# Kernel tuning notes

Hardware: AMD Instinct MI355X
Metric: run time of the kernel (lower is better)

Reference implementation:

```python
import jax, jax.numpy as jnp
import numpy as np

B, L, D, HD, DC = 2, 2048, 2048, 64, 2048
NH = D // HD  # 32 heads


def _rms_norm(x, eps):
    return x * jax.lax.rsqrt(jnp.mean(jnp.square(x), axis=-1, keepdims=True) + eps)


def _apply_rope(x, rope):
    # x: [b,h,l,d]; rope: [2,l,d]. x_hat = interleave(-x_odd, x_even)
    x2 = x.reshape(*x.shape[:-1], HD // 2, 2)
    x_hat = jnp.stack([-x2[..., 1], x2[..., 0]], axis=-1).reshape(x.shape)
    return x * rope[0] + x_hat * rope[1]


def setup_inputs() -> dict:
    key = jax.random.key(0)
    ks = jax.random.split(key, 6)
    return {
        "x": jax.random.normal(ks[0], (B, L, D), jnp.float32),
        "condition": jax.random.normal(ks[1], (B, DC), jnp.float32),
        "rope": jax.random.normal(ks[2], (2, L, HD), jnp.float32),
        "w_ada": jax.random.normal(ks[3], (2 * D, DC), jnp.float32) * 0.02,
        "w_qkv": jax.random.normal(ks[4], (3 * D, D), jnp.float32) * 0.02,
        "w_out": jax.random.normal(ks[5], (D, D), jnp.float32) * 0.02,
        "qk_w": jnp.ones((HD,), jnp.float32),
    }


def reference(x, condition, rope, w_ada, w_qkv, w_out, qk_w):
    eps = jnp.finfo(x.dtype).eps
    # AdaRMSNorm
    ss = (condition @ w_ada.T)[:, None, :]          # [b,1,2D]
    shift, scale = jnp.split(ss, 2, axis=-1)
    h = _rms_norm(x, eps) * (1.0 + scale) + shift   # [b,l,D]
    # fused QKV projection: 'b l (n h d)'
    qkv = (h @ w_qkv.T).reshape(B, L, 3, NH, HD)
    qkv = jnp.transpose(qkv, (2, 0, 3, 1, 4))       # [3,b,h,l,d]
    q, k, v = qkv[0], qkv[1], qkv[2]
    # per-head RMSNorm (with affine weight) + RoPE
    q = _apply_rope(_rms_norm(q, eps) * qk_w, rope)
    k = _apply_rope(_rms_norm(k, eps) * qk_w, rope)
    # SDPA
    scores = jnp.einsum('bhqd,bhkd->bhqk', q, k) / jnp.sqrt(jnp.asarray(HD, x.dtype))
    attn = jax.nn.softmax(scores, axis=-1)
    o = jnp.einsum('bhqk,bhkd->bhqd', attn, v)      # [b,h,l,d]
    o = jnp.transpose(o, (0, 2, 1, 3)).reshape(B, L, D)
    return o @ w_out.T
```

## Files before the change

### kernel.cpp

```cpp
#include <hip/hip_runtime.h>


typedef __bf16 bf16x8 __attribute__((ext_vector_type(8)));
typedef float  f32x4  __attribute__((ext_vector_type(4)));
typedef float  f32x16 __attribute__((ext_vector_type(16)));

#define EPS_F32 1.1920929e-07f
#define QSCALE 0.18033688011112042f

#if defined(__has_builtin)
#  if __has_builtin(__builtin_amdgcn_exp2f)
#    define EXP2F(x) __builtin_amdgcn_exp2f(x)
#  else
#    define EXP2F(x) __expf((x) * 0.6931471805599453f)
#  endif
#  if __has_builtin(__builtin_amdgcn_rcpf)
#    define RCPF(x) __builtin_amdgcn_rcpf(x)
#  else
#    define RCPF(x) (1.0f / (x))
#  endif
#else
#  define EXP2F(x) __expf((x) * 0.6931471805599453f)
#  define RCPF(x) (1.0f / (x))
#endif

__device__ __forceinline__ float bf2f(unsigned int u16) {
  union { unsigned int i; float f; } v; v.i = (u16 & 0xffffu) << 16; return v.f;
}
__device__ __forceinline__ unsigned short f2bf(float f) {
  union { float f; unsigned int i; } v; v.f = f;
  unsigned int r = v.i + 0x7fffu + ((v.i >> 16) & 1u);
  return (unsigned short)(r >> 16);
}
__device__ __forceinline__ unsigned int f2bf_rn_u(float f) {
  union { float f; unsigned int i; } v; v.f = f;
  return v.i + 0x8000u;
}

__device__ __forceinline__ void gload16(const void* g, void* l) {
  __builtin_amdgcn_global_load_lds(
      (const __attribute__((address_space(1))) unsigned int*)(unsigned long long)g,
      (__attribute__((address_space(3))) unsigned int*)(unsigned int)(unsigned long long)l,
      16, 0, 0);
}

__global__ __launch_bounds__(256) void ada_gemm_kernel(
    const float* __restrict__ cond, const float* __restrict__ w_ada,
    float* __restrict__ ss)
{
  const int lane = threadIdx.x & 63;
  const int gw = blockIdx.x * 4 + (threadIdx.x >> 6);
  const int b = gw >> 12;
  const int j = gw & 4095;
  const float4* wr = (const float4*)(w_ada + j * 2048);
  const float4* cr = (const float4*)(cond + b * 2048);
  float acc = 0.f;
  #pragma unroll
  for (int k4 = 0; k4 < 8; ++k4) {
    float4 w = wr[lane + k4 * 64];
    float4 c = cr[lane + k4 * 64];
    acc += w.x * c.x + w.y * c.y + w.z * c.z + w.w * c.w;
  }
  #pragma unroll
  for (int off = 1; off < 64; off <<= 1) acc += __shfl_xor(acc, off);
  if (lane == 0) ss[b * 4096 + j] = acc;
}

__global__ __launch_bounds__(256) void ada_rms_kernel(
    const float* __restrict__ x, const float* __restrict__ ss,
    unsigned short* __restrict__ H)
{
  const int row = blockIdx.x;
  const int b = row >> 11;
  const int tid = threadIdx.x;
  const int lane = tid & 63, wave = tid >> 6;
  const float* xr = x + (size_t)row * 2048;
  float4 v0 = ((const float4*)xr)[tid * 2];
  float4 v1 = ((const float4*)xr)[tid * 2 + 1];
  float ssq = v0.x*v0.x + v0.y*v0.y + v0.z*v0.z + v0.w*v0.w
            + v1.x*v1.x + v1.y*v1.y + v1.z*v1.z + v1.w*v1.w;
  #pragma unroll
  for (int off = 1; off < 64; off <<= 1) ssq += __shfl_xor(ssq, off);
  __shared__ float red[4];
  if (lane == 0) red[wave] = ssq;
  __syncthreads();
  const float tot = red[0] + red[1] + red[2] + red[3];
  const float r = rsqrtf(tot * (1.f / 2048.f) + EPS_F32);
  const int c0 = tid * 8;
  const float* sh = ss + b * 4096;
  float xv[8] = {v0.x, v0.y, v0.z, v0.w, v1.x, v1.y, v1.z, v1.w};
  unsigned int pk[4];
  #pragma unroll
  for (int p = 0; p < 4; ++p) {
    const int c = c0 + p * 2;
    float h0 = xv[p*2+0] * r * (1.f + sh[2048 + c])     + sh[c];
    float h1 = xv[p*2+1] * r * (1.f + sh[2048 + c + 1]) + sh[c + 1];
    pk[p] = (unsigned int)f2bf(h0) | ((unsigned int)f2bf(h1) << 16);
  }
  *(uint4*)&H[(size_t)row * 2048 + c0] = make_uint4(pk[0], pk[1], pk[2], pk[3]);
}

__global__ __launch_bounds__(256) void cast2_kernel(
    const float* __restrict__ a,
    const float* __restrict__ b,
    unsigned short* __restrict__ dst)
{
  const int i = blockIdx.x * 256 + threadIdx.x;
  float4 v = (i < 3145728) ? ((const float4*)a)[i]
                           : ((const float4*)b)[i - 3145728];
  unsigned int p0 = (unsigned int)f2bf(v.x) | ((unsigned int)f2bf(v.y) << 16);
  unsigned int p1 = (unsigned int)f2bf(v.z) | ((unsigned int)f2bf(v.w) << 16);
  *(uint2*)&dst[(size_t)i * 4] = make_uint2(p0, p1);
}

__global__ __launch_bounds__(512, 2) void gemm_qkv_8p(
    const unsigned short* __restrict__ A,
    const unsigned short* __restrict__ Bw,
    unsigned short* __restrict__ C,
    unsigned short* __restrict__ vt,
    const float* __restrict__ rope,
    const float* __restrict__ qk_w)
{
  __shared__ unsigned short As[2][2][8192];
  __shared__ unsigned short Bs[2][2][8192];

  const int tid  = threadIdx.x;
  const int lane = tid & 63;
  const int wave = tid >> 6;
  const int wrow = (wave >> 2) * 128;
  const int wcol = (wave & 3) * 64;

  const int swz = (blockIdx.x & 7) * 48 + (blockIdx.x >> 3);
  const int bx = swz >> 4;
  const int by = swz & 15;
  const int bm = by * 256;
  const int bn = bx * 256;

  const int fr = lane & 15;
  const int q_ = lane >> 4;
  const int laneoff = fr * 32 + ((q_ ^ ((fr >> 1) & 3)) << 3);

  const int rA  = wave * 32 + (lane >> 2);
  const int kk  = (lane & 3) ^ ((lane >> 3) & 3);
  const unsigned short* Ag0 = A  + (size_t)(bm + rA) * 2048 + kk * 8;
  const unsigned short* Ag1 = Ag0 + (size_t)16 * 2048;
  const unsigned short* Bg0 = Bw + (size_t)(bn + rA) * 2048 + kk * 8;
  const unsigned short* Bg1 = Bg0 + (size_t)16 * 2048;
  const int ldso = rA * 32 + (lane & 3) * 8;

  f32x4 acc[8][4] = {};
  bf16x8 fA[4], fB[4];

#define STAGE_A(SB, SKH, KT) do { \
    gload16(Ag0 + (KT) * 64 + (SKH) * 32, &As[SB][SKH][ldso]); \
    gload16(Ag1 + (KT) * 64 + (SKH) * 32, &As[SB][SKH][ldso + 512]); } while (0)
#define STAGE_B(SB, SKH, KT) do { \
    gload16(Bg0 + (KT) * 64 + (SKH) * 32, &Bs[SB][SKH][ldso]); \
    gload16(Bg1 + (KT) * 64 + (SKH) * 32, &Bs[SB][SKH][ldso + 512]); } while (0)
#define VMW(N) asm volatile("s_waitcnt vmcnt(" #N ")" ::: "memory")
#define LDB(BUF, KH) do { const unsigned short* p_ = &Bs[BUF][KH][wcol * 32 + laneoff]; \
    fB[0] = *(const bf16x8*)&p_[0];    fB[1] = *(const bf16x8*)&p_[512]; \
    fB[2] = *(const bf16x8*)&p_[1024]; fB[3] = *(const bf16x8*)&p_[1536]; } while (0)
#define LDA(BUF, KH, MH) do { const unsigned short* p_ = &As[BUF][KH][(wrow + (MH) * 64) * 32 + laneoff]; \
    fA[0] = *(const bf16x8*)&p_[0];    fA[1] = *(const bf16x8*)&p_[512]; \
    fA[2] = *(const bf16x8*)&p_[1024]; fA[3] = *(const bf16x8*)&p_[1536]; } while (0)
#define MFMA16(MH) do { \
    _Pragma("unroll") \
    for (int f_ = 0; f_ < 4; ++f_) { \
      _Pragma("unroll") \
      for (int n_ = 0; n_ < 4; ++n_) \
        acc[(MH) * 4 + f_][n_] = __builtin_amdgcn_mfma_f32_16x16x32_bf16( \
            fA[f_], fB[n_], acc[(MH) * 4 + f_][n_], 0, 0, 0); \
    } } while (0)
#define PH_MID() do { __builtin_amdgcn_s_barrier(); \
    asm volatile("s_waitcnt lgkmcnt(0)"); \
    __builtin_amdgcn_s_setprio(1); } while (0)
#define PH_END() do { __builtin_amdgcn_s_setprio(0); \
    __builtin_amdgcn_s_barrier(); } while (0)

  STAGE_A(0, 0, 0); STAGE_B(0, 0, 0); STAGE_A(0, 1, 0); STAGE_B(0, 1, 0);
  VMW(4);
  __builtin_amdgcn_s_barrier();

  for (int it = 0; it < 16; ++it) {
    const int t1 = 2 * it + 1;
    const int t2 = 2 * it + 2;
    const bool pf = (it < 15);

    LDB(0, 0); LDA(0, 0, 0);
    STAGE_A(1, 0, t1);
    PH_MID(); MFMA16(0); PH_END();
    LDA(0, 0, 1);
    STAGE_B(1, 0, t1);
    VMW(4);
    PH_MID(); MFMA16(1); PH_END();
    LDB(0, 1); LDA(0, 1, 0);
    STAGE_A(1, 1, t1);
    PH_MID(); MFMA16(0); PH_END();
    LDA(0, 1, 1);
    STAGE_B(1, 1, t1);
    VMW(4);
    PH_MID(); MFMA16(1); PH_END();

    LDB(1, 0); LDA(1, 0, 0);
    if (pf) STAGE_A(0, 0, t2);
    PH_MID(); MFMA16(0); PH_END();
    LDA(1, 0, 1);
    if (pf) { STAGE_B(0, 0, t2); VMW(4); }
    else    { VMW(0); }
    PH_MID(); MFMA16(1); PH_END();
    LDB(1, 1); LDA(1, 1, 0);
    if (pf) STAGE_A(0, 1, t2);
    PH_MID(); MFMA16(0); PH_END();
    LDA(1, 1, 1);
    if (pf) STAGE_B(0, 1, t2);
    VMW(4);
    PH_MID(); MFMA16(1); PH_END();
  }

#undef STAGE_A
#undef STAGE_B
#undef VMW
#undef LDB
#undef LDA
#undef MFMA16
#undef PH_MID
#undef PH_END

  const int cr = (lane >> 4) * 4;
  const int cc = lane & 15;
  if (bn >= 4096) {
    #pragma unroll
    for (int mf = 0; mf < 8; ++mf)
      #pragma unroll
      for (int nf = 0; nf < 4; ++nf)
        #pragma unroll
        for (int r = 0; r < 4; ++r) {
          const int m  = bm + wrow + mf * 16 + cr + r;
          const int dg = bn + wcol + nf * 16 + cc - 4096;
          const int l  = m & 2047;
          const size_t dst = ((size_t)((m >> 11) * 32 + (dg >> 6)) * 64 + (dg & 63)) * 2048
                           + (l >> 6) * 64 + (l & 15) * 4 + ((l >> 4) & 3);
          vt[dst] = f2bf(acc[mf][nf][r]);
        }
  } else {
    const bool is_q = (bn + wcol) < 2048;
    const float qs = is_q ? QSCALE : 1.0f;
    float w4[4];
    #pragma unroll
    for (int nf = 0; nf < 4; ++nf) w4[nf] = qk_w[nf * 16 + cc];
    #pragma unroll
    for (int mf = 0; mf < 8; ++mf)
      #pragma unroll
      for (int r = 0; r < 4; ++r) {
        const int row = bm + wrow + mf * 16 + cr + r;
        const int l = row & 2047;
        float ssq = 0.f;
        #pragma unroll
        for (int nf = 0; nf < 4; ++nf) { const float v = acc[mf][nf][r]; ssq += v * v; }
        ssq += __shfl_xor(ssq, 1);
        ssq += __shfl_xor(ssq, 2);
        ssq += __shfl_xor(ssq, 4);
        ssq += __shfl_xor(ssq, 8);
        const float rn = rsqrtf(ssq * (1.f / 64.f) + EPS_F32) * qs;
        const float* rp0 = rope + l * 64 + cc;
        const float* rp1 = rp0 + 131072;
        #pragma unroll
        for (int nf = 0; nf < 4; ++nf) {
          const float vn = acc[mf][nf][r] * rn * w4[nf];
          const float vp = __shfl_xor(vn, 1);
          const float vh = (cc & 1) ? vp : -vp;
          const float o = vn * rp0[nf * 16] + vh * rp1[nf * 16];
          C[(size_t)row * 6144 + bn + wcol + nf * 16 + cc] = f2bf(o);
        }
      }
  }
}

__global__ __launch_bounds__(512, 1) void gemm_out_4p(
    const unsigned short* __restrict__ A,
    const unsigned short* __restrict__ Bw,
    float* __restrict__ C)
{
  __shared__ unsigned short As[2][2][8192];
  __shared__ unsigned short Bs[2][2][4096];

  const int tid  = threadIdx.x;
  const int lane = tid & 63;
  const int wave = tid >> 6;
  const int wrow = (wave >> 1) * 64;
  const int wcol = (wave & 1) * 64;

  const int swz = (blockIdx.x & 7) * 32 + (blockIdx.x >> 3);
  const int bx = swz >> 4;
  const int by = swz & 15;
  const int bm = by * 256;
  const int bn = bx * 128;

  const int fr = lane & 15;
  const int q_ = lane >> 4;
  const int laneoff = fr * 32 + ((q_ ^ ((fr >> 1) & 3)) << 3);

  const int rA = wave * 32 + (lane >> 2);
  const int rB = wave * 16 + (lane >> 2);
  const int kk = (lane & 3) ^ ((lane >> 3) & 3);
  const unsigned short* Ag0 = A  + (size_t)(bm + rA) * 2048 + kk * 8;
  const unsigned short* Ag1 = Ag0 + (size_t)16 * 2048;
  const unsigned short* Bg0 = Bw + (size_t)(bn + rB) * 2048 + kk * 8;
  const int ldsoA = rA * 32 + (lane & 3) * 8;
  const int ldsoB = rB * 32 + (lane & 3) * 8;

  f32x4 acc[4][4] = {};
  bf16x8 fA[4], fB[4];

#define STAGE_A4(SB, SKH, KT) do { \
    gload16(Ag0 + (KT) * 64 + (SKH) * 32, &As[SB][SKH][ldsoA]); \
    gload16(Ag1 + (KT) * 64 + (SKH) * 32, &As[SB][SKH][ldsoA + 512]); } while (0)
#define STAGE_B4(SB, SKH, KT) \
    gload16(Bg0 + (KT) * 64 + (SKH) * 32, &Bs[SB][SKH][ldsoB])
#define VMW(N) asm volatile("s_waitcnt vmcnt(" #N ")" ::: "memory")
#define LDB4(BUF, KH) do { const unsigned short* p_ = &Bs[BUF][KH][wcol * 32 + laneoff]; \
    fB[0] = *(const bf16x8*)&p_[0];    fB[1] = *(const bf16x8*)&p_[512]; \
    fB[2] = *(const bf16x8*)&p_[1024]; fB[3] = *(const bf16x8*)&p_[1536]; } while (0)
#define LDA4(BUF, KH) do { const unsigned short* p_ = &As[BUF][KH][wrow * 32 + laneoff]; \
    fA[0] = *(const bf16x8*)&p_[0];    fA[1] = *(const bf16x8*)&p_[512]; \
    fA[2] = *(const bf16x8*)&p_[1024]; fA[3] = *(const bf16x8*)&p_[1536]; } while (0)
#define MFMA16_4() do { \
    _Pragma("unroll") \
    for (int f_ = 0; f_ < 4; ++f_) { \
      _Pragma("unroll") \
      for (int n_ = 0; n_ < 4; ++n_) \
        acc[f_][n_] = __builtin_amdgcn_mfma_f32_16x16x32_bf16( \
            fA[f_], fB[n_], acc[f_][n_], 0, 0, 0); \
    } } while (0)
#define PH_MID() do { __builtin_amdgcn_s_barrier(); \
    asm volatile("s_waitcnt lgkmcnt(0)"); \
    __builtin_amdgcn_s_setprio(1); } while (0)
#define PH_END() do { __builtin_amdgcn_s_setprio(0); \
    __builtin_amdgcn_s_barrier(); } while (0)

  STAGE_A4(0, 0, 0); STAGE_B4(0, 0, 0);
  STAGE_A4(0, 1, 0); STAGE_B4(0, 1, 0);
  VMW(3);
  __builtin_amdgcn_s_barrier();

  for (int it = 0; it < 16; ++it) {
    const int t1 = 2 * it + 1;
    const int t2 = 2 * it + 2;
    const bool pf = (it < 15);

    LDB4(0, 0); LDA4(0, 0);
    STAGE_A4(1, 0, t1); STAGE_B4(1, 0, t1);
    VMW(3);
    PH_MID(); MFMA16_4(); PH_END();
    LDB4(0, 1); LDA4(0, 1);
    STAGE_A4(1, 1, t1); STAGE_B4(1, 1, t1);
    VMW(3);
    PH_MID(); MFMA16_4(); PH_END();

    LDB4(1, 0); LDA4(1, 0);
    if (pf) { STAGE_A4(0, 0, t2); STAGE_B4(0, 0, t2); VMW(3); }
    else    { VMW(0); }
    PH_MID(); MFMA16_4(); PH_END();
    LDB4(1, 1); LDA4(1, 1);
    if (pf) { STAGE_A4(0, 1, t2); STAGE_B4(0, 1, t2); VMW(3); }
    else    { VMW(0); }
    PH_MID(); MFMA16_4(); PH_END();
  }

#undef STAGE_A4
#undef STAGE_B4
#undef VMW
#undef LDB4
#undef LDA4
#undef MFMA16_4
#undef PH_MID
#undef PH_END

  const int cr = (lane >> 4) * 4;
  const int cc = lane & 15;
  #pragma unroll
  for (int f = 0; f < 4; ++f)
    #pragma unroll
    for (int n = 0; n < 4; ++n)
      #pragma unroll
      for (int r = 0; r < 4; ++r) {
        const int row = bm + wrow + f * 16 + cr + r;
        const int col = bn + wcol + n * 16 + cc;
        C[(size_t)row * 2048 + col] = acc[f][n][r];
      }
}

__global__ __launch_bounds__(256, 2) void attn_mfma_kernel(
    const unsigned short* __restrict__ QKV,
    const unsigned short* __restrict__ Vt,
    unsigned short* __restrict__ O)
{
  __shared__ unsigned short Ks[64 * 72];
  __shared__ unsigned short Vs[64 * 72];
  __shared__ unsigned short Ps[4 * 64 * 68];
  const int tid  = threadIdx.x;
  const int lane = tid & 63;
  const int wave = tid >> 6;
  const int blk = blockIdx.x;
  const int bh = blk & 63;
  const int qt = blk >> 6;
  const int b = bh >> 5, h = bh & 31;
  const int rowbase = b << 11;
  const int qbase = qt * 256 + wave * 64;

  const int m16  = lane & 15;
  const int quad = lane >> 4;
  const int m32  = lane & 31;
  const int hl   = lane >> 5;

  bf16x8 qf[4][2];
  #pragma unroll
  for (int qi = 0; qi < 4; ++qi)
    #pragma unroll
    for (int ch = 0; ch < 2; ++ch)
      qf[qi][ch] = *(const bf16x8*)&QKV[(size_t)(rowbase + qbase + qi * 16 + m16) * 6144
                                        + h * 64 + ch * 32 + quad * 8];

  const int sr = tid >> 2;
  const int sc = (tid & 3) * 16;
  const unsigned short* Kg = QKV + (size_t)(rowbase + sr) * 6144 + 2048 + h * 64 + sc;
  const unsigned short* Vg = Vt + (size_t)(bh * 64 + sr) * 2048 + sc;

  f32x16 accO[2][2] = {};
  float part[4][4] = {};
  unsigned short* Pw = &Ps[(wave * 64) * 68];

  for (int kt = 0; kt < 32; ++kt) {
    __syncthreads();
    {
      const uint4* kp = (const uint4*)(Kg + (size_t)kt * 64 * 6144);
      const uint4* vp = (const uint4*)(Vg + kt * 64);
      uint4 k0 = kp[0], k1 = kp[1];
      uint4 v0 = vp[0], v1 = vp[1];
      *(uint4*)&Ks[sr * 72 + sc]     = k0;
      *(uint4*)&Ks[sr * 72 + sc + 8] = k1;
      *(uint4*)&Vs[sr * 72 + sc]     = v0;
      *(uint4*)&Vs[sr * 72 + sc + 8] = v1;
    }
    __syncthreads();

    unsigned int pk[4][4][2];
    #pragma unroll
    for (int kj = 0; kj < 4; ++kj) {
      bf16x8 kf0 = *(const bf16x8*)&Ks[(kj * 16 + m16) * 72 + quad * 8];
      bf16x8 kf1 = *(const bf16x8*)&Ks[(kj * 16 + m16) * 72 + 32 + quad * 8];
      #pragma unroll
      for (int qi = 0; qi < 4; ++qi) {
        f32x4 acc = {};
        acc = __builtin_amdgcn_mfma_f32_16x16x32_bf16(qf[qi][0], kf0, acc, 0, 0, 0);
        acc = __builtin_amdgcn_mfma_f32_16x16x32_bf16(qf[qi][1], kf1, acc, 0, 0, 0);
        #pragma unroll
        for (int r = 0; r < 4; ++r) {
          float p = EXP2F(acc[r]);
          part[qi][r] += p;
          unsigned int pb = f2bf_rn_u(p);
          if (kj == 0)      pk[qi][r][0]  = pb >> 16;
          else if (kj == 1) pk[qi][r][0] |= pb & 0xffff0000u;
          else if (kj == 2) pk[qi][r][1]  = pb >> 16;
          else              pk[qi][r][1] |= pb & 0xffff0000u;
        }
      }
    }
    #pragma unroll
    for (int qi = 0; qi < 4; ++qi)
      #pragma unroll
      for (int r = 0; r < 4; ++r)
        *(uint2*)&Pw[(qi * 16 + quad * 4 + r) * 68 + m16 * 4] =
            make_uint2(pk[qi][r][0], pk[qi][r][1]);

    #pragma unroll
    for (int ch = 0; ch < 4; ++ch) {
      bf16x8 pa0 = *(const bf16x8*)&Pw[m32 * 68 + ch * 16 + hl * 8];
      bf16x8 pa1 = *(const bf16x8*)&Pw[(32 + m32) * 68 + ch * 16 + hl * 8];
      bf16x8 vb0 = *(const bf16x8*)&Vs[m32 * 72 + ch * 16 + hl * 8];
      bf16x8 vb1 = *(const bf16x8*)&Vs[(32 + m32) * 72 + ch * 16 + hl * 8];
      accO[0][0] = __builtin_amdgcn_mfma_f32_32x32x16_bf16(pa0, vb0, accO[0][0], 0, 0, 0);
      accO[0][1] = __builtin_amdgcn_mfma_f32_32x32x16_bf16(pa0, vb1, accO[0][1], 0, 0, 0);
      accO[1][0] = __builtin_amdgcn_mfma_f32_32x32x16_bf16(pa1, vb0, accO[1][0], 0, 0, 0);
      accO[1][1] = __builtin_amdgcn_mfma_f32_32x32x16_bf16(pa1, vb1, accO[1][1], 0, 0, 0);
    }
  }

  #pragma unroll
  for (int qi = 0; qi < 4; ++qi)
    #pragma unroll
    for (int r = 0; r < 4; ++r)
      #pragma unroll
      for (int off = 1; off < 16; off <<= 1)
        part[qi][r] += __shfl_xor(part[qi][r], off);

  #pragma unroll
  for (int qs = 0; qs < 2; ++qs) {
    #pragma unroll
    for (int reg = 0; reg < 16; ++reg) {
      const int r = reg & 3;
      const int s = reg >> 2;
      const int qsrc = ((2 * s + hl) & 3) * 16 + m16;
      const float rs = __shfl(part[qs * 2 + (reg >> 3)][r], qsrc);
      const float inv = RCPF(rs);
      const int rho = r + 8 * s + 4 * hl;
      const size_t base = (size_t)(rowbase + qbase + qs * 32 + rho) * 2048 + h * 64;
      O[base + m32]      = f2bf(accO[qs][0][reg] * inv);
      O[base + 32 + m32] = f2bf(accO[qs][1][reg] * inv);
    }
  }
}

extern "C" void kernel_launch(void* const* d_in, const int* in_sizes, int n_in,
                              void* d_out, int out_size, void* d_ws, size_t ws_size,
                              hipStream_t stream) {
  (void)in_sizes; (void)n_in; (void)out_size; (void)ws_size;
  const float* x     = (const float*)d_in[0];
  const float* cond  = (const float*)d_in[1];
  const float* rope  = (const float*)d_in[2];
  const float* w_ada = (const float*)d_in[3];
  const float* w_qkv = (const float*)d_in[4];
  const float* w_out = (const float*)d_in[5];
  const float* qk_w  = (const float*)d_in[6];
  float* out = (float*)d_out;

  char* ws = (char*)d_ws;
  float*          ss   = (float*)ws;
  unsigned short* H    = (unsigned short*)(ws + 32768);
  unsigned short* Wq   = H + 8388608;
  unsigned short* Wo   = Wq + 12582912;
  unsigned short* QKV  = Wo + 4194304;
  unsigned short* Vt_g = QKV + 25165824;

  ada_gemm_kernel<<<2048, 256, 0, stream>>>(cond, w_ada, ss);
  ada_rms_kernel<<<4096, 256, 0, stream>>>(x, ss, H);
  cast2_kernel<<<16384, 256, 0, stream>>>(w_qkv, w_out, Wq);
  gemm_qkv_8p<<<384, 512, 0, stream>>>(H, Wq, QKV, Vt_g, rope, qk_w);
  attn_mfma_kernel<<<512, 256, 0, stream>>>(QKV, Vt_g, H);
  gemm_out_4p<<<256, 512, 0, stream>>>(H, Wo, out);
}
```

Measured before the change: 447.6 us.

## Split QKV GEMM into 256x128 tiles and move QK norm+RoPE to separate kernel

Replaces the 256x256-tile QKV GEMM (two blocks per CU) with a 256x128-tile variant modeled on the out-projection kernel, launched with 768 blocks and a rescaled swizzle. The per-head RMSNorm, qk weight, scale and RoPE epilogue is moved out of the GEMM into a new elementwise kernel that rewrites Q and K in place. The goal is more blocks and a lighter GEMM epilogue, at the cost of an extra launch and an extra read and write of Q and K. Q/K are normalized from bf16-rounded values rather than fp32 accumulators, which slightly changes numerics.

Result: no change. 443.7 us (-0.9%).

```diff
diff --git a/kernel.cpp b/kernel.cpp
--- a/kernel.cpp
+++ b/kernel.cpp
@@ -27,6 +27,9 @@
 __device__ __forceinline__ float bf2f(unsigned int u16) {
   union { unsigned int i; float f; } v; v.i = (u16 & 0xffffu) << 16; return v.f;
 }
+__device__ __forceinline__ float bf2f_hi(unsigned int u32) {
+  union { unsigned int i; float f; } v; v.i = u32 & 0xffff0000u; return v.f;
+}
 __device__ __forceinline__ unsigned short f2bf(float f) {
   union { float f; unsigned int i; } v; v.f = f;
   unsigned int r = v.i + 0x7fffu + ((v.i >> 16) & 1u);
@@ -113,174 +116,11 @@
   *(uint2*)&dst[(size_t)i * 4] = make_uint2(p0, p1);
 }
 
-__global__ __launch_bounds__(512, 2) void gemm_qkv_8p(
+__global__ __launch_bounds__(512, 1) void gemm_qkv_4p(
     const unsigned short* __restrict__ A,
     const unsigned short* __restrict__ Bw,
     unsigned short* __restrict__ C,
-    unsigned short* __restrict__ vt,
-    const float* __restrict__ rope,
-    const float* __restrict__ qk_w)
-{
-  __shared__ unsigned short As[2][2][8192];
-  __shared__ unsigned short Bs[2][2][8192];
-
-  const int tid  = threadIdx.x;
-  const int lane = tid & 63;
-  const int wave = tid >> 6;
-  const int wrow = (wave >> 2) * 128;
-  const int wcol = (wave & 3) * 64;
-
-  const int swz = (blockIdx.x & 7) * 48 + (blockIdx.x >> 3);
-  const int bx = swz >> 4;
-  const int by = swz & 15;
-  const int bm = by * 256;
-  const int bn = bx * 256;
-
-  const int fr = lane & 15;
-  const int q_ = lane >> 4;
-  const int laneoff = fr * 32 + ((q_ ^ ((fr >> 1) & 3)) << 3);
-
-  const int rA  = wave * 32 + (lane >> 2);
-  const int kk  = (lane & 3) ^ ((lane >> 3) & 3);
-  const unsigned short* Ag0 = A  + (size_t)(bm + rA) * 2048 + kk * 8;
-  const unsigned short* Ag1 = Ag0 + (size_t)16 * 2048;
-  const unsigned short* Bg0 = Bw + (size_t)(bn + rA) * 2048 + kk * 8;
-  const unsigned short* Bg1 = Bg0 + (size_t)16 * 2048;
-  const int ldso = rA * 32 + (lane & 3) * 8;
-
-  f32x4 acc[8][4] = {};
-  bf16x8 fA[4], fB[4];
-
-#define STAGE_A(SB, SKH, KT) do { \
-    gload16(Ag0 + (KT) * 64 + (SKH) * 32, &As[SB][SKH][ldso]); \
-    gload16(Ag1 + (KT) * 64 + (SKH) * 32, &As[SB][SKH][ldso + 512]); } while (0)
-#define STAGE_B(SB, SKH, KT) do { \
-    gload16(Bg0 + (KT) * 64 + (SKH) * 32, &Bs[SB][SKH][ldso]); \
-    gload16(Bg1 + (KT) * 64 + (SKH) * 32, &Bs[SB][SKH][ldso + 512]); } while (0)
-#define VMW(N) asm volatile("s_waitcnt vmcnt(" #N ")" ::: "memory")
-#define LDB(BUF, KH) do { const unsigned short* p_ = &Bs[BUF][KH][wcol * 32 + laneoff]; \
-    fB[0] = *(const bf16x8*)&p_[0];    fB[1] = *(const bf16x8*)&p_[512]; \
-    fB[2] = *(const bf16x8*)&p_[1024]; fB[3] = *(const bf16x8*)&p_[1536]; } while (0)
-#define LDA(BUF, KH, MH) do { const unsigned short* p_ = &As[BUF][KH][(wrow + (MH) * 64) * 32 + laneoff]; \
-    fA[0] = *(const bf16x8*)&p_[0];    fA[1] = *(const bf16x8*)&p_[512]; \
-    fA[2] = *(const bf16x8*)&p_[1024]; fA[3] = *(const bf16x8*)&p_[1536]; } while (0)
-#define MFMA16(MH) do { \
-    _Pragma("unroll") \
-    for (int f_ = 0; f_ < 4; ++f_) { \
-      _Pragma("unroll") \
-      for (int n_ = 0; n_ < 4; ++n_) \
-        acc[(MH) * 4 + f_][n_] = __builtin_amdgcn_mfma_f32_16x16x32_bf16( \
-            fA[f_], fB[n_], acc[(MH) * 4 + f_][n_], 0, 0, 0); \
-    } } while (0)
-#define PH_MID() do { __builtin_amdgcn_s_barrier(); \
-    asm volatile("s_waitcnt lgkmcnt(0)"); \
-    __builtin_amdgcn_s_setprio(1); } while (0)
-#define PH_END() do { __builtin_amdgcn_s_setprio(0); \
-    __builtin_amdgcn_s_barrier(); } while (0)
-
-  STAGE_A(0, 0, 0); STAGE_B(0, 0, 0); STAGE_A(0, 1, 0); STAGE_B(0, 1, 0);
-  VMW(4);
-  __builtin_amdgcn_s_barrier();
-
-  for (int it = 0; it < 16; ++it) {
-    const int t1 = 2 * it + 1;
-    const int t2 = 2 * it + 2;
-    const bool pf = (it < 15);
-
-    LDB(0, 0); LDA(0, 0, 0);
-    STAGE_A(1, 0, t1);
-    PH_MID(); MFMA16(0); PH_END();
-    LDA(0, 0, 1);
-    STAGE_B(1, 0, t1);
-    VMW(4);
-    PH_MID(); MFMA16(1); PH_END();
-    LDB(0, 1); LDA(0, 1, 0);
-    STAGE_A(1, 1, t1);
-    PH_MID(); MFMA16(0); PH_END();
-    LDA(0, 1, 1);
-    STAGE_B(1, 1, t1);
-    VMW(4);
-    PH_MID(); MFMA16(1); PH_END();
-
-    LDB(1, 0); LDA(1, 0, 0);
-    if (pf) STAGE_A(0, 0, t2);
-    PH_MID(); MFMA16(0); PH_END();
-    LDA(1, 0, 1);
-    if (pf) { STAGE_B(0, 0, t2); VMW(4); }
-    else    { VMW(0); }
-    PH_MID(); MFMA16(1); PH_END();
-    LDB(1, 1); LDA(1, 1, 0);
-    if (pf) STAGE_A(0, 1, t2);
-    PH_MID(); MFMA16(0); PH_END();
-    LDA(1, 1, 1);
-    if (pf) STAGE_B(0, 1, t2);
-    VMW(4);
-    PH_MID(); MFMA16(1); PH_END();
-  }
-
-#undef STAGE_A
-#undef STAGE_B
-#undef VMW
-#undef LDB
-#undef LDA
-#undef MFMA16
-#undef PH_MID
-#undef PH_END
-
-  const int cr = (lane >> 4) * 4;
-  const int cc = lane & 15;
-  if (bn >= 4096) {
-    #pragma unroll
-    for (int mf = 0; mf < 8; ++mf)
-      #pragma unroll
-      for (int nf = 0; nf < 4; ++nf)
-        #pragma unroll
-        for (int r = 0; r < 4; ++r) {
-          const int m  = bm + wrow + mf * 16 + cr + r;
-          const int dg = bn + wcol + nf * 16 + cc - 4096;
-          const int l  = m & 2047;
-          const size_t dst = ((size_t)((m >> 11) * 32 + (dg >> 6)) * 64 + (dg & 63)) * 2048
-                           + (l >> 6) * 64 + (l & 15) * 4 + ((l >> 4) & 3);
-          vt[dst] = f2bf(acc[mf][nf][r]);
-        }
-  } else {
-    const bool is_q = (bn + wcol) < 2048;
-    const float qs = is_q ? QSCALE : 1.0f;
-    float w4[4];
-    #pragma unroll
-    for (int nf = 0; nf < 4; ++nf) w4[nf] = qk_w[nf * 16 + cc];
-    #pragma unroll
-    for (int mf = 0; mf < 8; ++mf)
-      #pragma unroll
-      for (int r = 0; r < 4; ++r) {
-        const int row = bm + wrow + mf * 16 + cr + r;
-        const int l = row & 2047;
-        float ssq = 0.f;
-        #pragma unroll
-        for (int nf = 0; nf < 4; ++nf) { const float v = acc[mf][nf][r]; ssq += v * v; }
-        ssq += __shfl_xor(ssq, 1);
-        ssq += __shfl_xor(ssq, 2);
-        ssq += __shfl_xor(ssq, 4);
-        ssq += __shfl_xor(ssq, 8);
-        const float rn = rsqrtf(ssq * (1.f / 64.f) + EPS_F32) * qs;
-        const float* rp0 = rope + l * 64 + cc;
-        const float* rp1 = rp0 + 131072;
-        #pragma unroll
-        for (int nf = 0; nf < 4; ++nf) {
-          const float vn = acc[mf][nf][r] * rn * w4[nf];
-          const float vp = __shfl_xor(vn, 1);
-          const float vh = (cc & 1) ? vp : -vp;
-          const float o = vn * rp0[nf * 16] + vh * rp1[nf * 16];
-          C[(size_t)row * 6144 + bn + wcol + nf * 16 + cc] = f2bf(o);
-        }
-      }
-  }
-}
-
-__global__ __launch_bounds__(512, 1) void gemm_out_4p(
-    const unsigned short* __restrict__ A,
-    const unsigned short* __restrict__ Bw,
-    float* __restrict__ C)
+    unsigned short* __restrict__ vt)
 {
   __shared__ unsigned short As[2][2][8192];
   __shared__ unsigned short Bs[2][2][4096];
@@ -291,7 +131,7 @@
   const int wrow = (wave >> 1) * 64;
   const int wcol = (wave & 1) * 64;
 
-  const int swz = (blockIdx.x & 7) * 32 + (blockIdx.x >> 3);
+  const int swz = (blockIdx.x & 7) * 96 + (blockIdx.x >> 3);
   const int bx = swz >> 4;
   const int by = swz & 15;
   const int bm = by * 256;
@@ -379,6 +219,136 @@
 
   const int cr = (lane >> 4) * 4;
   const int cc = lane & 15;
+  if (bn >= 4096) {
+    #pragma unroll
+    for (int mf = 0; mf < 4; ++mf)
+      #pragma unroll
+      for (int nf = 0; nf < 4; ++nf)
+        #pragma unroll
+        for (int r = 0; r < 4; ++r) {
+          const int m  = bm + wrow + mf * 16 + cr + r;
+          const int dg = bn + wcol + nf * 16 + cc - 4096;
+          const int l  = m & 2047;
+          const size_t dst = ((size_t)((m >> 11) * 32 + (dg >> 6)) * 64 + (dg & 63)) * 2048
+                           + (l >> 6) * 64 + (l & 15) * 4 + ((l >> 4) & 3);
+          vt[dst] = f2bf(acc[mf][nf][r]);
+        }
+  } else {
+    #pragma unroll
+    for (int mf = 0; mf < 4; ++mf)
+      #pragma unroll
+      for (int nf = 0; nf < 4; ++nf)
+        #pragma unroll
+        for (int r = 0; r < 4; ++r) {
+          const int row = bm + wrow + mf * 16 + cr + r;
+          const int col = bn + wcol + nf * 16 + cc;
+          C[(size_t)row * 6144 + col] = f2bf(acc[mf][nf][r]);
+        }
+  }
+}
+
+__global__ __launch_bounds__(512, 1) void gemm_out_4p(
+    const unsigned short* __restrict__ A,
+    const unsigned short* __restrict__ Bw,
+    float* __restrict__ C)
+{
+  __shared__ unsigned short As[2][2][8192];
+  __shared__ unsigned short Bs[2][2][4096];
+
+  const int tid  = threadIdx.x;
+  const int lane = tid & 63;
+  const int wave = tid >> 6;
+  const int wrow = (wave >> 1) * 64;
+  const int wcol = (wave & 1) * 64;
+
+  const int swz = (blockIdx.x & 7) * 32 + (blockIdx.x >> 3);
+  const int bx = swz >> 4;
+  const int by = swz & 15;
+  const int bm = by * 256;
+  const int bn = bx * 128;
+
+  const int fr = lane & 15;
+  const int q_ = lane >> 4;
+  const int laneoff = fr * 32 + ((q_ ^ ((fr >> 1) & 3)) << 3);
+
+  const int rA = wave * 32 + (lane >> 2);
+  const int rB = wave * 16 + (lane >> 2);
+  const int kk = (lane & 3) ^ ((lane >> 3) & 3);
+  const unsigned short* Ag0 = A  + (size_t)(bm + rA) * 2048 + kk * 8;
+  const unsigned short* Ag1 = Ag0 + (size_t)16 * 2048;
+  const unsigned short* Bg0 = Bw + (size_t)(bn + rB) * 2048 + kk * 8;
+  const int ldsoA = rA * 32 + (lane & 3) * 8;
+  const int ldsoB = rB * 32 + (lane & 3) * 8;
+
+  f32x4 acc[4][4] = {};
+  bf16x8 fA[4], fB[4];
+
+#define STAGE_A4(SB, SKH, KT) do { \
+    gload16(Ag0 + (KT) * 64 + (SKH) * 32, &As[SB][SKH][ldsoA]); \
+    gload16(Ag1 + (KT) * 64 + (SKH) * 32, &As[SB][SKH][ldsoA + 512]); } while (0)
+#define STAGE_B4(SB, SKH, KT) \
+    gload16(Bg0 + (KT) * 64 + (SKH) * 32, &Bs[SB][SKH][ldsoB])
+#define VMW(N) asm volatile("s_waitcnt vmcnt(" #N ")" ::: "memory")
+#define LDB4(BUF, KH) do { const unsigned short* p_ = &Bs[BUF][KH][wcol * 32 + laneoff]; \
+    fB[0] = *(const bf16x8*)&p_[0];    fB[1] = *(const bf16x8*)&p_[512]; \
+    fB[2] = *(const bf16x8*)&p_[1024]; fB[3] = *(const bf16x8*)&p_[1536]; } while (0)
+#define LDA4(BUF, KH) do { const unsigned short* p_ = &As[BUF][KH][wrow * 32 + laneoff]; \
+    fA[0] = *(const bf16x8*)&p_[0];    fA[1] = *(const bf16x8*)&p_[512]; \
+    fA[2] = *(const bf16x8*)&p_[1024]; fA[3] = *(const bf16x8*)&p_[1536]; } while (0)
+#define MFMA16_4() do { \
+    _Pragma("unroll") \
+    for (int f_ = 0; f_ < 4; ++f_) { \
+      _Pragma("unroll") \
+      for (int n_ = 0; n_ < 4; ++n_) \
+        acc[f_][n_] = __builtin_amdgcn_mfma_f32_16x16x32_bf16( \
+            fA[f_], fB[n_], acc[f_][n_], 0, 0, 0); \
+    } } while (0)
+#define PH_MID() do { __builtin_amdgcn_s_barrier(); \
+    asm volatile("s_waitcnt lgkmcnt(0)"); \
+    __builtin_amdgcn_s_setprio(1); } while (0)
+#define PH_END() do { __builtin_amdgcn_s_setprio(0); \
+    __builtin_amdgcn_s_barrier(); } while (0)
+
+  STAGE_A4(0, 0, 0); STAGE_B4(0, 0, 0);
+  STAGE_A4(0, 1, 0); STAGE_B4(0, 1, 0);
+  VMW(3);
+  __builtin_amdgcn_s_barrier();
+
+  for (int it = 0; it < 16; ++it) {
+    const int t1 = 2 * it + 1;
+    const int t2 = 2 * it + 2;
+    const bool pf = (it < 15);
+
+    LDB4(0, 0); LDA4(0, 0);
+    STAGE_A4(1, 0, t1); STAGE_B4(1, 0, t1);
+    VMW(3);
+    PH_MID(); MFMA16_4(); PH_END();
+    LDB4(0, 1); LDA4(0, 1);
+    STAGE_A4(1, 1, t1); STAGE_B4(1, 1, t1);
+    VMW(3);
+    PH_MID(); MFMA16_4(); PH_END();
+
+    LDB4(1, 0); LDA4(1, 0);
+    if (pf) { STAGE_A4(0, 0, t2); STAGE_B4(0, 0, t2); VMW(3); }
+    else    { VMW(0); }
+    PH_MID(); MFMA16_4(); PH_END();
+    LDB4(1, 1); LDA4(1, 1);
+    if (pf) { STAGE_A4(0, 1, t2); STAGE_B4(0, 1, t2); VMW(3); }
+    else    { VMW(0); }
+    PH_MID(); MFMA16_4(); PH_END();
+  }
+
+#undef STAGE_A4
+#undef STAGE_B4
+#undef VMW
+#undef LDB4
+#undef LDA4
+#undef MFMA16_4
+#undef PH_MID
+#undef PH_END
+
+  const int cr = (lane >> 4) * 4;
+  const int cc = lane & 15;
   #pragma unroll
   for (int f = 0; f < 4; ++f)
     #pragma unroll
@@ -389,6 +359,66 @@
         const int col = bn + wcol + n * 16 + cc;
         C[(size_t)row * 2048 + col] = acc[f][n][r];
       }
+}
+
+__global__ __launch_bounds__(256) void qk_rope_kernel(
+    unsigned short* __restrict__ QKV, const float* __restrict__ rope,
+    const float* __restrict__ qk_w)
+{
+  const int tid  = threadIdx.x;
+  const int lane = tid & 63;
+  const int task = blockIdx.x * 4 + (tid >> 6);
+  const int hg   = task & 3;
+  const int bl   = task >> 2;
+  const int l    = bl & 2047;
+  const int h    = hg * 8 + (lane >> 3);
+  const int d0   = (lane & 7) * 8;
+  const size_t base = (size_t)bl * 6144 + h * 64 + d0;
+
+  float r0[8], r1[8], wv[8];
+  {
+    const float4* p0 = (const float4*)(rope + l * 64 + d0);
+    const float4* p1 = (const float4*)(rope + 131072 + l * 64 + d0);
+    const float4* pw = (const float4*)(qk_w + d0);
+    float4 a, b2;
+    a = p0[0]; b2 = p0[1];
+    r0[0]=a.x; r0[1]=a.y; r0[2]=a.z; r0[3]=a.w; r0[4]=b2.x; r0[5]=b2.y; r0[6]=b2.z; r0[7]=b2.w;
+    a = p1[0]; b2 = p1[1];
+    r1[0]=a.x; r1[1]=a.y; r1[2]=a.z; r1[3]=a.w; r1[4]=b2.x; r1[5]=b2.y; r1[6]=b2.z; r1[7]=b2.w;
+    a = pw[0]; b2 = pw[1];
+    wv[0]=a.x; wv[1]=a.y; wv[2]=a.z; wv[3]=a.w; wv[4]=b2.x; wv[5]=b2.y; wv[6]=b2.z; wv[7]=b2.w;
+  }
+
+  #pragma unroll
+  for (int t = 0; t < 2; ++t) {
+    unsigned short* p = &QKV[base + (size_t)2048 * t];
+    const uint4 raw = *(const uint4*)p;
+    const unsigned int* u = (const unsigned int*)&raw;
+    float v[8];
+    #pragma unroll
+    for (int j = 0; j < 4; ++j) {
+      v[2*j]   = bf2f(u[j]);
+      v[2*j+1] = bf2f_hi(u[j]);
+    }
+    float sq = v[0]*v[0] + v[1]*v[1] + v[2]*v[2] + v[3]*v[3]
+             + v[4]*v[4] + v[5]*v[5] + v[6]*v[6] + v[7]*v[7];
+    sq += __shfl_xor(sq, 1);
+    sq += __shfl_xor(sq, 2);
+    sq += __shfl_xor(sq, 4);
+    const float rn = rsqrtf(sq * (1.f / 64.f) + EPS_F32)
+                   * ((t == 0) ? QSCALE : 1.0f);
+    float vn[8];
+    #pragma unroll
+    for (int j = 0; j < 8; ++j) vn[j] = v[j] * (rn * wv[j]);
+    unsigned int pk[4];
+    #pragma unroll
+    for (int j = 0; j < 4; ++j) {
+      const float o0 = vn[2*j]   * r0[2*j]   - vn[2*j+1] * r1[2*j];
+      const float o1 = vn[2*j+1] * r0[2*j+1] + vn[2*j]   * r1[2*j+1];
+      pk[j] = (unsigned int)f2bf(o0) | ((unsigned int)f2bf(o1) << 16);
+    }
+    *(uint4*)p = make_uint4(pk[0], pk[1], pk[2], pk[3]);
+  }
 }
 
 __global__ __launch_bounds__(256, 2) void attn_mfma_kernel(
@@ -536,7 +566,8 @@
   ada_gemm_kernel<<<2048, 256, 0, stream>>>(cond, w_ada, ss);
   ada_rms_kernel<<<4096, 256, 0, stream>>>(x, ss, H);
   cast2_kernel<<<16384, 256, 0, stream>>>(w_qkv, w_out, Wq);
-  gemm_qkv_8p<<<384, 512, 0, stream>>>(H, Wq, QKV, Vt_g, rope, qk_w);
+  gemm_qkv_4p<<<768, 512, 0, stream>>>(H, Wq, QKV, Vt_g);
+  qk_rope_kernel<<<4096, 256, 0, stream>>>(QKV, rope, qk_w);
   attn_mfma_kernel<<<512, 256, 0, stream>>>(QKV, Vt_g, H);
   gemm_out_4p<<<256, 512, 0, stream>>>(H, Wo, out);
 }
```
